# Kernel optimization log

Measured on AMD Instinct MI355X. Metric: run time of the kernel, lower is better.

The kernel has to match this reference:

```python
import jax, jax.numpy as jnp
import numpy as np

DIM = 2048        # model hidden size
INTER = 1408      # per-expert intermediate size
E = 16            # n_routed_experts
TOPK = 2          # n_activated_experts
S_INTER = 2816    # shared experts intermediate (n_shared_experts * INTER)
T = 4096          # tokens (batch*seq, module flattens to [-1, dim])
ROUTE_SCALE = 1.0


def setup_inputs() -> dict:
    key = jax.random.key(0)
    ks = jax.random.split(key, 8)
    g = lambda k, shape, scale: (jax.random.normal(k, shape, dtype=jnp.float32) * scale)
    return {
        "x": g(ks[0], (T, DIM), 1.0),
        "gate_w": g(ks[1], (E, DIM), 0.02),
        "w1": g(ks[2], (E, INTER, DIM), 0.02),
        "w2": g(ks[3], (E, DIM, INTER), 0.02),
        "w3": g(ks[4], (E, INTER, DIM), 0.02),
        "sw1": g(ks[5], (S_INTER, DIM), 0.02),
        "sw2": g(ks[6], (DIM, S_INTER), 0.02),
        "sw3": g(ks[7], (S_INTER, DIM), 0.02),
    }


def _moe_forward(x, gate_w, w1, w2, w3, sw1, sw2, sw3):
    t = x.shape[0]
    # ---- gate: softmax scores -> top-k experts per token ----
    scores = jax.nn.softmax(x @ gate_w.T, axis=-1)          # [T, E]
    top_w, top_i = jax.lax.top_k(scores, TOPK)              # [T, K]
    top_w = top_w * ROUTE_SCALE
    # dense combine weights [T, E]: zero for unselected experts
    combine = jnp.zeros((t, E), x.dtype).at[jnp.arange(t)[:, None], top_i].add(top_w)
    # ---- routed experts: gated silu MLP per expert, weighted combine ----
    # loop over the small fixed expert count; tokens with combine==0 contribute 0,
    # matching the original scatter/gather dispatch math exactly.
    y = jnp.zeros_like(x)
    for e in range(E):
        h = jax.nn.silu(x @ w1[e].T) * (x @ w3[e].T)        # [T, INTER]
        y = y + (h @ w2[e].T) * combine[:, e:e + 1]
    # ---- shared experts ----
    z = (jax.nn.silu(x @ sw1.T) * (x @ sw3.T)) @ sw2.T      # [T, DIM]
    return y + z


def reference(x, gate_w, w1, w2, w3, sw1, sw2, sw3):
    return _moe_forward(x, gate_w, w1, w2, w3, sw1, sw2, sw3)
```

## Files before the change

kernel.cpp:

```cpp
#include <hip/hip_runtime.h>
#include <hip/hip_bf16.h>
#include <cstdint>
#include <cstddef>

#define TTOK   4096
#define DIM_   2048
#define INTER_ 1408
#define NEXP   16
#define SINTER_ 2816
#define BM 128
#define BN 128
#define BK 32
#define MAXROWS (TTOK*2 + NEXP*BM)
#define MAXMT   (TTOK*2/BM + NEXP)

typedef unsigned short u16;
typedef __attribute__((ext_vector_type(8))) short short8;
typedef __attribute__((ext_vector_type(4))) float f32x4;

__device__ __forceinline__ u16 f2bf(float f) {
    __hip_bfloat16 h = __float2bfloat16(f);
    union { __hip_bfloat16 h; u16 u; } c; c.h = h; return c.u;
}

__device__ __forceinline__ unsigned pk2(float a, float b) {
    unsigned r;
    asm("v_cvt_pk_bf16_f32 %0, %1, %2" : "=v"(r) : "v"(a), "v"(b));
    return r;
}

__device__ __forceinline__ int4 pack8(float4 a, float4 b) {
    int4 r;
    r.x = (int)pk2(a.x, a.y);
    r.y = (int)pk2(a.z, a.w);
    r.z = (int)pk2(b.x, b.y);
    r.w = (int)pk2(b.z, b.w);
    return r;
}


__global__ void init_kernel(int* perm_rt, float* pw_rt, int* perm_sh, int* misc) {
    int i = blockIdx.x * 256 + threadIdx.x;
    if (i < MAXROWS) { perm_rt[i] = -1; pw_rt[i] = 0.f; }
    if (i < TTOK)    perm_sh[i] = i;
    if (i < 32)      misc[i] = 0;
}

__global__ void convert_x_kernel(const float* __restrict__ x, u16* __restrict__ xb) {
    size_t i = (size_t)blockIdx.x * 256 + threadIdx.x;
    float4 v = *(const float4*)(x + i * 4);
    uint2 o;
    o.x = pk2(v.x, v.y);
    o.y = pk2(v.z, v.w);
    *(uint2*)(xb + i * 4) = o;
}

__global__ void gate_kernel(const float* __restrict__ x, const float* __restrict__ gw,
                            int* __restrict__ topi, float* __restrict__ topw,
                            int* __restrict__ misc) {
    int t = blockIdx.x;
    int lane = threadIdx.x;
    const float* xr = x + (size_t)t * DIM_;
    float acc[NEXP];
#pragma unroll
    for (int e = 0; e < NEXP; e++) acc[e] = 0.f;
#pragma unroll
    for (int i = 0; i < 8; i++) {
        int k = i * 256 + lane * 4;
        float4 xv = *(const float4*)(xr + k);
#pragma unroll
        for (int e = 0; e < NEXP; e++) {
            float4 gv = *(const float4*)(gw + (size_t)e * DIM_ + k);
            acc[e] += xv.x * gv.x + xv.y * gv.y + xv.z * gv.z + xv.w * gv.w;
        }
    }
#pragma unroll
    for (int e = 0; e < NEXP; e++) {
        float v = acc[e];
        for (int off = 32; off > 0; off >>= 1) v += __shfl_down(v, off);
        acc[e] = v;
    }
    if (lane == 0) {
        float m = acc[0];
#pragma unroll
        for (int e = 1; e < NEXP; e++) m = fmaxf(m, acc[e]);
        float p[NEXP]; float s = 0.f;
#pragma unroll
        for (int e = 0; e < NEXP; e++) { p[e] = __expf(acc[e] - m); s += p[e]; }
        int i0 = 0; float v0 = p[0];
#pragma unroll
        for (int e = 1; e < NEXP; e++) if (p[e] > v0) { v0 = p[e]; i0 = e; }
        int i1 = -1; float v1 = -1.f;
#pragma unroll
        for (int e = 0; e < NEXP; e++) if (e != i0 && p[e] > v1) { v1 = p[e]; i1 = e; }
        float inv = 1.f / s;
        topi[2 * t] = i0; topi[2 * t + 1] = i1;
        topw[2 * t] = v0 * inv; topw[2 * t + 1] = v1 * inv;
        atomicAdd(&misc[i0], 1);
        atomicAdd(&misc[i1], 1);
    }
}

__global__ void scan_kernel(int* misc) {
    int* counts = misc;
    int* base   = misc + 32;
    int* te     = misc + 48;
    int* tr     = misc + 128;
    int b = 0, tt = 0;
    for (int e = 0; e < NEXP; e++) {
        int c = counts[e];
        int nt = (c + BM - 1) >> 7;
        base[e] = b;
        for (int i = 0; i < nt; i++) { te[tt] = e; tr[tt] = b + i * BM; tt++; }
        b += nt * BM;
    }
    for (int i = tt; i < MAXMT; i++) te[i] = -1;
}

__global__ void scatter_kernel(const int* __restrict__ topi, const float* __restrict__ topw,
                               int* __restrict__ misc, int* __restrict__ perm,
                               float* __restrict__ pw) {
    int t = blockIdx.x * 256 + threadIdx.x;
    if (t >= TTOK) return;
    int* fill = misc + 16;
    int* base = misc + 32;
#pragma unroll
    for (int k = 0; k < 2; k++) {
        int e = topi[2 * t + k];
        int pos = base[e] + atomicAdd(&fill[e], 1);
        perm[pos] = t;
        pw[pos] = topw[2 * t + k];
    }
}


template<bool GROUPED>
__global__ __launch_bounds__(256, 2) void gemm_h13_k(
    const u16* __restrict__ Xb,
    const float* __restrict__ W1b, const float* __restrict__ W3b,
    u16* __restrict__ H,
    const int* __restrict__ perm,
    const int* __restrict__ te, const int* __restrict__ tr,
    int N, int K, int nt_m, int chunk)
{
    const int q = (blockIdx.x & 7) * chunk + (blockIdx.x >> 3);
    if (q >= nt_m * (N / BN)) return;
    const int jn = q / nt_m, im = q % nt_m;
    int e, slot0;
    if (GROUPED) { e = te[im]; if (e < 0) return; slot0 = tr[im]; }
    else         { e = 0; slot0 = im * BM; }
    const int n0 = jn * BN;
    const float* W1 = W1b + (size_t)e * N * K;
    const float* W3 = W3b + (size_t)e * N * K;

    __shared__ __align__(16) u16 As[BM * BK];
    __shared__ __align__(16) u16 B1s[BM * BK];
    __shared__ __align__(16) u16 B3s[BM * BK];

    const int tid = threadIdx.x;
    const int lane = tid & 63, wid = tid >> 6;
    const int wr = wid >> 1, wc = wid & 1;
    const int col = lane & 15, kg = lane >> 4;

    const int r0 = tid >> 2, ko = (tid & 3) * 8;
    const int tok0 = perm[slot0 + r0];
    const int tok1 = perm[slot0 + r0 + 64];
    const u16* pA0 = (tok0 >= 0) ? Xb + (size_t)tok0 * K + ko : nullptr;
    const u16* pA1 = (tok1 >= 0) ? Xb + (size_t)tok1 * K + ko : nullptr;
    const int rB = tid >> 1, hfB = (tid & 1) * 16;
    const float* p1 = W1 + (size_t)(n0 + rB) * K + hfB;
    const float* p3 = W3 + (size_t)(n0 + rB) * K + hfB;

    f32x4 acc1[4][4] = {};
    f32x4 acc3[4][4] = {};

    int4 va0, va1;
    float4 f1[4], f3[4];

    va0 = pA0 ? *(const int4*)(pA0) : make_int4(0, 0, 0, 0);
    va1 = pA1 ? *(const int4*)(pA1) : make_int4(0, 0, 0, 0);
#pragma unroll
    for (int i = 0; i < 4; i++) { f1[i] = *(const float4*)(p1 + i * 4); f3[i] = *(const float4*)(p3 + i * 4); }

    for (int k0 = 0; k0 < K; k0 += BK) {
        *(int4*)(As + r0 * BK + ko) = va0;
        *(int4*)(As + (r0 + 64) * BK + ko) = va1;
        *(int4*)(B1s + rB * BK + hfB)     = pack8(f1[0], f1[1]);
        *(int4*)(B1s + rB * BK + hfB + 8) = pack8(f1[2], f1[3]);
        *(int4*)(B3s + rB * BK + hfB)     = pack8(f3[0], f3[1]);
        *(int4*)(B3s + rB * BK + hfB + 8) = pack8(f3[2], f3[3]);
        __syncthreads();

        const int kn = k0 + BK;
        if (kn < K) {
            va0 = pA0 ? *(const int4*)(pA0 + kn) : make_int4(0, 0, 0, 0);
            va1 = pA1 ? *(const int4*)(pA1 + kn) : make_int4(0, 0, 0, 0);
#pragma unroll
            for (int i = 0; i < 4; i++) {
                f1[i] = *(const float4*)(p1 + kn + i * 4);
                f3[i] = *(const float4*)(p3 + kn + i * 4);
            }
        }

        short8 a[4];
#pragma unroll
        for (int mi = 0; mi < 4; mi++)
            a[mi] = *(const short8*)(As + (wr * 64 + mi * 16 + col) * BK + kg * 8);
#pragma unroll
        for (int ni = 0; ni < 4; ni++) {
            short8 v1 = *(const short8*)(B1s + (wc * 64 + ni * 16 + col) * BK + kg * 8);
            short8 v3 = *(const short8*)(B3s + (wc * 64 + ni * 16 + col) * BK + kg * 8);
#pragma unroll
            for (int mi = 0; mi < 4; mi++) {
                acc1[mi][ni] = __builtin_amdgcn_mfma_f32_16x16x32_bf16(a[mi], v1, acc1[mi][ni], 0, 0, 0);
                acc3[mi][ni] = __builtin_amdgcn_mfma_f32_16x16x32_bf16(a[mi], v3, acc3[mi][ni], 0, 0, 0);
            }
        }
        __syncthreads();
    }

#pragma unroll
    for (int mi = 0; mi < 4; mi++) {
#pragma unroll
        for (int j = 0; j < 4; j++) {
            int row = slot0 + wr * 64 + mi * 16 + kg * 4 + j;
#pragma unroll
            for (int ni = 0; ni < 4; ni++) {
                float v1 = acc1[mi][ni][j];
                float v3 = acc3[mi][ni][j];
                float hv = v1 / (1.f + __expf(-v1)) * v3;
                int c = n0 + wc * 64 + ni * 16 + col;
                H[(size_t)row * N + c] = f2bf(hv);
            }
        }
    }
}

template<bool ATOMIC>
__global__ __launch_bounds__(256, 2) void gemm_out_k(
    const u16* __restrict__ Hm,
    const float* __restrict__ W2b,
    float* __restrict__ Out,
    const int* __restrict__ perm, const float* __restrict__ pw,
    const int* __restrict__ te, const int* __restrict__ tr,
    int K, int nt_m, int chunk)
{
    const int q = (blockIdx.x & 7) * chunk + (blockIdx.x >> 3);
    if (q >= nt_m * (DIM_ / BN)) return;
    const int jn = q / nt_m, im = q % nt_m;
    int e, slot0;
    if (ATOMIC) { e = te[im]; if (e < 0) return; slot0 = tr[im]; }
    else        { e = 0; slot0 = im * BM; }
    const int n0 = jn * BN;
    const float* W2 = W2b + (size_t)e * DIM_ * K;

    __shared__ __align__(16) u16 As[BM * BK];
    __shared__ __align__(16) u16 Bs[BM * BK];

    const int tid = threadIdx.x;
    const int lane = tid & 63, wid = tid >> 6;
    const int wr = wid >> 1, wc = wid & 1;
    const int col = lane & 15, kg = lane >> 4;

    const int r0 = tid >> 2, ko = (tid & 3) * 8;
    const int rB = tid >> 1, hfB = (tid & 1) * 16;
    const u16* pA0 = Hm + (size_t)(slot0 + r0) * K + ko;
    const u16* pA1 = Hm + (size_t)(slot0 + r0 + 64) * K + ko;
    const float* p2 = W2 + (size_t)(n0 + rB) * K + hfB;

    f32x4 acc[4][4] = {};

    int4 va0, va1;
    float4 fb[4];
    va0 = *(const int4*)(pA0);
    va1 = *(const int4*)(pA1);
#pragma unroll
    for (int i = 0; i < 4; i++) fb[i] = *(const float4*)(p2 + i * 4);

    for (int k0 = 0; k0 < K; k0 += BK) {
        *(int4*)(As + r0 * BK + ko) = va0;
        *(int4*)(As + (r0 + 64) * BK + ko) = va1;
        *(int4*)(Bs + rB * BK + hfB)     = pack8(fb[0], fb[1]);
        *(int4*)(Bs + rB * BK + hfB + 8) = pack8(fb[2], fb[3]);
        __syncthreads();

        const int kn = k0 + BK;
        if (kn < K) {
            va0 = *(const int4*)(pA0 + kn);
            va1 = *(const int4*)(pA1 + kn);
#pragma unroll
            for (int i = 0; i < 4; i++) fb[i] = *(const float4*)(p2 + kn + i * 4);
        }

        short8 a[4];
#pragma unroll
        for (int mi = 0; mi < 4; mi++)
            a[mi] = *(const short8*)(As + (wr * 64 + mi * 16 + col) * BK + kg * 8);
#pragma unroll
        for (int ni = 0; ni < 4; ni++) {
            short8 bv = *(const short8*)(Bs + (wc * 64 + ni * 16 + col) * BK + kg * 8);
#pragma unroll
            for (int mi = 0; mi < 4; mi++)
                acc[mi][ni] = __builtin_amdgcn_mfma_f32_16x16x32_bf16(a[mi], bv, acc[mi][ni], 0, 0, 0);
        }
        __syncthreads();
    }

#pragma unroll
    for (int mi = 0; mi < 4; mi++) {
#pragma unroll
        for (int j = 0; j < 4; j++) {
            int rloc = wr * 64 + mi * 16 + kg * 4 + j;
            int slot = slot0 + rloc;
            if (ATOMIC) {
                int token = perm[slot];
                if (token < 0) continue;
                float w = pw[slot];
#pragma unroll
                for (int ni = 0; ni < 4; ni++) {
                    int c = n0 + wc * 64 + ni * 16 + col;
                    atomicAdd(&Out[(size_t)token * DIM_ + c], acc[mi][ni][j] * w);
                }
            } else {
#pragma unroll
                for (int ni = 0; ni < 4; ni++) {
                    int c = n0 + wc * 64 + ni * 16 + col;
                    Out[(size_t)slot * DIM_ + c] = acc[mi][ni][j];
                }
            }
        }
    }
}


extern "C" void kernel_launch(void* const* d_in, const int* in_sizes, int n_in,
                              void* d_out, int out_size, void* d_ws, size_t ws_size,
                              hipStream_t stream) {
    (void)in_sizes; (void)n_in; (void)out_size; (void)ws_size;
    const float* x   = (const float*)d_in[0];
    const float* gw  = (const float*)d_in[1];
    const float* w1  = (const float*)d_in[2];
    const float* w2  = (const float*)d_in[3];
    const float* w3  = (const float*)d_in[4];
    const float* sw1 = (const float*)d_in[5];
    const float* sw2 = (const float*)d_in[6];
    const float* sw3 = (const float*)d_in[7];
    float* out = (float*)d_out;

    char* ws = (char*)d_ws;
    size_t off = 0;
    auto take = [&](size_t bytes) -> void* {
        void* p = ws + off;
        off += (bytes + 255) & ~(size_t)255;
        return p;
    };
    u16*   xb      = (u16*)take((size_t)TTOK * DIM_ * 2);
    u16*   hbuf    = (u16*)take((size_t)MAXROWS * INTER_ * 2);
    int*   perm_rt = (int*)take((size_t)MAXROWS * 4);
    float* pw_rt   = (float*)take((size_t)MAXROWS * 4);
    int*   perm_sh = (int*)take((size_t)TTOK * 4);
    int*   topi    = (int*)take((size_t)TTOK * 2 * 4);
    float* topw    = (float*)take((size_t)TTOK * 2 * 4);
    int*   misc    = (int*)take(1024);

    init_kernel<<<MAXROWS / 256, 256, 0, stream>>>(perm_rt, pw_rt, perm_sh, misc);
    convert_x_kernel<<<(TTOK * DIM_ / 4) / 256, 256, 0, stream>>>(x, xb);
    gate_kernel<<<TTOK, 64, 0, stream>>>(x, gw, topi, topw, misc);
    scan_kernel<<<1, 1, 0, stream>>>(misc);
    scatter_kernel<<<TTOK / 256, 256, 0, stream>>>(topi, topw, misc, perm_rt, pw_rt);

    auto grid8 = [](int total) { return ((total + 7) / 8) * 8; };
    auto chunk8 = [](int total) { return (total + 7) / 8; };

    {
        int total = (TTOK / BM) * (SINTER_ / BN);
        gemm_h13_k<false><<<grid8(total), 256, 0, stream>>>(
            xb, sw1, sw3, hbuf, perm_sh, nullptr, nullptr, SINTER_, DIM_, TTOK / BM, chunk8(total));
    }
    {
        int total = (TTOK / BM) * (DIM_ / BN);
        gemm_out_k<false><<<grid8(total), 256, 0, stream>>>(
            hbuf, sw2, out, nullptr, nullptr, nullptr, nullptr, SINTER_, TTOK / BM, chunk8(total));
    }
    {
        int total = MAXMT * (INTER_ / BN);
        gemm_h13_k<true><<<grid8(total), 256, 0, stream>>>(
            xb, w1, w3, hbuf, perm_rt, misc + 48, misc + 128, INTER_, DIM_, MAXMT, chunk8(total));
    }
    {
        int total = MAXMT * (DIM_ / BN);
        gemm_out_k<true><<<grid8(total), 256, 0, stream>>>(
            hbuf, w2, out, perm_rt, pw_rt, misc + 48, misc + 128, INTER_, MAXMT, chunk8(total));
    }
}
```

Before: 868.7 us.

## Pre-convert weights to bf16 and stage GEMM tiles via global_load_lds

Adds a bulk pass that converts all expert and shared weights from fp32 to bf16 in workspace on every call. New GEMM kernels then read bf16 weights and use global_load_lds to copy A/B tiles straight into shared memory, replacing the register-staged fp32 load and in-loop pack. A zero row stands in for padded tokens so the direct loads never need a null check. The weight conversion adds a full fp32 read plus bf16 write of every weight on each call. The new loop is single-buffered with no prefetch overlap, and the old fp32 path is kept as a fallback when the workspace is too small.

```diff
diff --git a/kernel.cpp b/kernel.cpp
--- a/kernel.cpp
+++ b/kernel.cpp
@@ -18,6 +18,13 @@
 typedef __attribute__((ext_vector_type(8))) short short8;
 typedef __attribute__((ext_vector_type(4))) float f32x4;
 
+#define AS3P(p) ((__attribute__((address_space(3))) void*)(p))
+#define AS1P(p) ((const __attribute__((address_space(1))) void*)(p))
+
+__device__ __forceinline__ void gll16(const u16* g, u16* l) {
+    __builtin_amdgcn_global_load_lds(AS1P(g), AS3P(l), 16, 0, 0);
+}
+
 __device__ __forceinline__ u16 f2bf(float f) {
     __hip_bfloat16 h = __float2bfloat16(f);
     union { __hip_bfloat16 h; u16 u; } c; c.h = h; return c.u;
@@ -39,20 +46,21 @@
 }
 
 
-__global__ void init_kernel(int* perm_rt, float* pw_rt, int* perm_sh, int* misc) {
+__global__ void init_kernel(int* perm_rt, float* pw_rt, int* perm_sh, int* misc, int* zrow) {
     int i = blockIdx.x * 256 + threadIdx.x;
     if (i < MAXROWS) { perm_rt[i] = -1; pw_rt[i] = 0.f; }
     if (i < TTOK)    perm_sh[i] = i;
     if (i < 32)      misc[i] = 0;
-}
-
-__global__ void convert_x_kernel(const float* __restrict__ x, u16* __restrict__ xb) {
-    size_t i = (size_t)blockIdx.x * 256 + threadIdx.x;
-    float4 v = *(const float4*)(x + i * 4);
-    uint2 o;
-    o.x = pk2(v.x, v.y);
-    o.y = pk2(v.z, v.w);
-    *(uint2*)(xb + i * 4) = o;
+    if (i < 1024)    zrow[i] = 0;
+}
+
+__global__ void cvt_kernel(const float* __restrict__ s, u16* __restrict__ d, int n8) {
+    int stride = gridDim.x * 256;
+    for (int i = blockIdx.x * 256 + threadIdx.x; i < n8; i += stride) {
+        const float4* s4 = (const float4*)(s + (size_t)i * 8);
+        float4 a = s4[0], b = s4[1];
+        *(int4*)(d + (size_t)i * 8) = pack8(a, b);
+    }
 }
 
 __global__ void gate_kernel(const float* __restrict__ x, const float* __restrict__ gw,
@@ -136,6 +144,185 @@
 
 template<bool GROUPED>
 __global__ __launch_bounds__(256, 2) void gemm_h13_k(
+    const u16* __restrict__ Xb,
+    const u16* __restrict__ W1b, const u16* __restrict__ W3b,
+    u16* __restrict__ H,
+    const int* __restrict__ perm,
+    const int* __restrict__ te, const int* __restrict__ tr,
+    const u16* __restrict__ zrow,
+    int N, int K, int nt_m, int chunk)
+{
+    const int q = (blockIdx.x & 7) * chunk + (blockIdx.x >> 3);
+    if (q >= nt_m * (N / BN)) return;
+    const int jn = q / nt_m, im = q % nt_m;
+    int e, slot0;
+    if (GROUPED) { e = te[im]; if (e < 0) return; slot0 = tr[im]; }
+    else         { e = 0; slot0 = im * BM; }
+    const int n0 = jn * BN;
+    const u16* W1 = W1b + (size_t)e * N * K;
+    const u16* W3 = W3b + (size_t)e * N * K;
+
+    __shared__ __align__(16) u16 As[BM * BK];
+    __shared__ __align__(16) u16 B1s[BM * BK];
+    __shared__ __align__(16) u16 B3s[BM * BK];
+
+    const int tid = threadIdx.x;
+    const int lane = tid & 63, wid = tid >> 6;
+    const int wr = wid >> 1, wc = wid & 1;
+    const int col = lane & 15, kg = lane >> 4;
+
+    const int lr = lane >> 2, kb = (lane & 3) * 8;
+    const int ar0 = wid * 32 + lr, ar1 = ar0 + 16;
+    const int ta0 = perm[slot0 + ar0];
+    const int ta1 = perm[slot0 + ar1];
+    const u16* ga0 = (ta0 >= 0 ? Xb + (size_t)ta0 * K : zrow) + kb;
+    const u16* ga1 = (ta1 >= 0 ? Xb + (size_t)ta1 * K : zrow) + kb;
+    const u16* gb1a = W1 + (size_t)(n0 + ar0) * K + kb;
+    const u16* gb1b = W1 + (size_t)(n0 + ar1) * K + kb;
+    const u16* gb3a = W3 + (size_t)(n0 + ar0) * K + kb;
+    const u16* gb3b = W3 + (size_t)(n0 + ar1) * K + kb;
+    u16* la0 = As  + (wid * 32) * BK;
+    u16* la1 = As  + (wid * 32 + 16) * BK;
+    u16* lb1a = B1s + (wid * 32) * BK;
+    u16* lb1b = B1s + (wid * 32 + 16) * BK;
+    u16* lb3a = B3s + (wid * 32) * BK;
+    u16* lb3b = B3s + (wid * 32 + 16) * BK;
+
+    f32x4 acc1[4][4] = {};
+    f32x4 acc3[4][4] = {};
+
+    for (int k0 = 0; k0 < K; k0 += BK) {
+        gll16(ga0 + k0, la0);
+        gll16(ga1 + k0, la1);
+        gll16(gb1a + k0, lb1a);
+        gll16(gb1b + k0, lb1b);
+        gll16(gb3a + k0, lb3a);
+        gll16(gb3b + k0, lb3b);
+        __syncthreads();
+
+        short8 a[4];
+#pragma unroll
+        for (int mi = 0; mi < 4; mi++)
+            a[mi] = *(const short8*)(As + (wr * 64 + mi * 16 + col) * BK + kg * 8);
+#pragma unroll
+        for (int ni = 0; ni < 4; ni++) {
+            short8 v1 = *(const short8*)(B1s + (wc * 64 + ni * 16 + col) * BK + kg * 8);
+            short8 v3 = *(const short8*)(B3s + (wc * 64 + ni * 16 + col) * BK + kg * 8);
+#pragma unroll
+            for (int mi = 0; mi < 4; mi++) {
+                acc1[mi][ni] = __builtin_amdgcn_mfma_f32_16x16x32_bf16(a[mi], v1, acc1[mi][ni], 0, 0, 0);
+                acc3[mi][ni] = __builtin_amdgcn_mfma_f32_16x16x32_bf16(a[mi], v3, acc3[mi][ni], 0, 0, 0);
+            }
+        }
+        __syncthreads();
+    }
+
+#pragma unroll
+    for (int mi = 0; mi < 4; mi++) {
+#pragma unroll
+        for (int j = 0; j < 4; j++) {
+            int row = slot0 + wr * 64 + mi * 16 + kg * 4 + j;
+#pragma unroll
+            for (int ni = 0; ni < 4; ni++) {
+                float v1 = acc1[mi][ni][j];
+                float v3 = acc3[mi][ni][j];
+                float hv = v1 / (1.f + __expf(-v1)) * v3;
+                int c = n0 + wc * 64 + ni * 16 + col;
+                H[(size_t)row * N + c] = f2bf(hv);
+            }
+        }
+    }
+}
+
+template<bool ATOMIC>
+__global__ __launch_bounds__(256, 2) void gemm_out_k(
+    const u16* __restrict__ Hm,
+    const u16* __restrict__ W2b,
+    float* __restrict__ Out,
+    const int* __restrict__ perm, const float* __restrict__ pw,
+    const int* __restrict__ te, const int* __restrict__ tr,
+    int K, int nt_m, int chunk)
+{
+    const int q = (blockIdx.x & 7) * chunk + (blockIdx.x >> 3);
+    if (q >= nt_m * (DIM_ / BN)) return;
+    const int jn = q / nt_m, im = q % nt_m;
+    int e, slot0;
+    if (ATOMIC) { e = te[im]; if (e < 0) return; slot0 = tr[im]; }
+    else        { e = 0; slot0 = im * BM; }
+    const int n0 = jn * BN;
+    const u16* W2 = W2b + (size_t)e * DIM_ * K;
+
+    __shared__ __align__(16) u16 As[BM * BK];
+    __shared__ __align__(16) u16 Bs[BM * BK];
+
+    const int tid = threadIdx.x;
+    const int lane = tid & 63, wid = tid >> 6;
+    const int wr = wid >> 1, wc = wid & 1;
+    const int col = lane & 15, kg = lane >> 4;
+
+    const int lr = lane >> 2, kb = (lane & 3) * 8;
+    const int ar0 = wid * 32 + lr, ar1 = ar0 + 16;
+    const u16* ga0 = Hm + (size_t)(slot0 + ar0) * K + kb;
+    const u16* ga1 = Hm + (size_t)(slot0 + ar1) * K + kb;
+    const u16* gb0 = W2 + (size_t)(n0 + ar0) * K + kb;
+    const u16* gb1 = W2 + (size_t)(n0 + ar1) * K + kb;
+    u16* la0 = As + (wid * 32) * BK;
+    u16* la1 = As + (wid * 32 + 16) * BK;
+    u16* lb0 = Bs + (wid * 32) * BK;
+    u16* lb1 = Bs + (wid * 32 + 16) * BK;
+
+    f32x4 acc[4][4] = {};
+
+    for (int k0 = 0; k0 < K; k0 += BK) {
+        gll16(ga0 + k0, la0);
+        gll16(ga1 + k0, la1);
+        gll16(gb0 + k0, lb0);
+        gll16(gb1 + k0, lb1);
+        __syncthreads();
+
+        short8 a[4];
+#pragma unroll
+        for (int mi = 0; mi < 4; mi++)
+            a[mi] = *(const short8*)(As + (wr * 64 + mi * 16 + col) * BK + kg * 8);
+#pragma unroll
+        for (int ni = 0; ni < 4; ni++) {
+            short8 bv = *(const short8*)(Bs + (wc * 64 + ni * 16 + col) * BK + kg * 8);
+#pragma unroll
+            for (int mi = 0; mi < 4; mi++)
+                acc[mi][ni] = __builtin_amdgcn_mfma_f32_16x16x32_bf16(a[mi], bv, acc[mi][ni], 0, 0, 0);
+        }
+        __syncthreads();
+    }
+
+#pragma unroll
+    for (int mi = 0; mi < 4; mi++) {
+#pragma unroll
+        for (int j = 0; j < 4; j++) {
+            int rloc = wr * 64 + mi * 16 + kg * 4 + j;
+            int slot = slot0 + rloc;
+            if (ATOMIC) {
+                int token = perm[slot];
+                if (token < 0) continue;
+                float w = pw[slot];
+#pragma unroll
+                for (int ni = 0; ni < 4; ni++) {
+                    int c = n0 + wc * 64 + ni * 16 + col;
+                    atomicAdd(&Out[(size_t)token * DIM_ + c], acc[mi][ni][j] * w);
+                }
+            } else {
+#pragma unroll
+                for (int ni = 0; ni < 4; ni++) {
+                    int c = n0 + wc * 64 + ni * 16 + col;
+                    Out[(size_t)slot * DIM_ + c] = acc[mi][ni][j];
+                }
+            }
+        }
+    }
+}
+
+
+template<bool GROUPED>
+__global__ __launch_bounds__(256, 2) void gemm_h13_f32(
     const u16* __restrict__ Xb,
     const float* __restrict__ W1b, const float* __restrict__ W3b,
     u16* __restrict__ H,
@@ -176,7 +363,6 @@
 
     int4 va0, va1;
     float4 f1[4], f3[4];
-
     va0 = pA0 ? *(const int4*)(pA0) : make_int4(0, 0, 0, 0);
     va1 = pA1 ? *(const int4*)(pA1) : make_int4(0, 0, 0, 0);
 #pragma unroll
@@ -237,7 +423,7 @@
 }
 
 template<bool ATOMIC>
-__global__ __launch_bounds__(256, 2) void gemm_out_k(
+__global__ __launch_bounds__(256, 2) void gemm_out_f32(
     const u16* __restrict__ Hm,
     const float* __restrict__ W2b,
     float* __restrict__ Out,
@@ -336,7 +522,7 @@
 extern "C" void kernel_launch(void* const* d_in, const int* in_sizes, int n_in,
                               void* d_out, int out_size, void* d_ws, size_t ws_size,
                               hipStream_t stream) {
-    (void)in_sizes; (void)n_in; (void)out_size; (void)ws_size;
+    (void)in_sizes; (void)n_in; (void)out_size;
     const float* x   = (const float*)d_in[0];
     const float* gw  = (const float*)d_in[1];
     const float* w1  = (const float*)d_in[2];
@@ -362,9 +548,21 @@
     int*   topi    = (int*)take((size_t)TTOK * 2 * 4);
     float* topw    = (float*)take((size_t)TTOK * 2 * 4);
     int*   misc    = (int*)take(1024);
-
-    init_kernel<<<MAXROWS / 256, 256, 0, stream>>>(perm_rt, pw_rt, perm_sh, misc);
-    convert_x_kernel<<<(TTOK * DIM_ / 4) / 256, 256, 0, stream>>>(x, xb);
+    int*   zrow    = (int*)take(4096);
+    const size_t nW  = (size_t)NEXP * INTER_ * DIM_;
+    const size_t nSW = (size_t)SINTER_ * DIM_;
+    size_t common_end = off;
+    u16* w1b  = (u16*)take(nW * 2);
+    u16* w2b  = (u16*)take(nW * 2);
+    u16* w3b  = (u16*)take(nW * 2);
+    u16* sw1b = (u16*)take(nSW * 2);
+    u16* sw2b = (u16*)take(nSW * 2);
+    u16* sw3b = (u16*)take(nSW * 2);
+    const bool fast = (off <= ws_size);
+    (void)common_end;
+
+    init_kernel<<<MAXROWS / 256, 256, 0, stream>>>(perm_rt, pw_rt, perm_sh, misc, zrow);
+    cvt_kernel<<<2048, 256, 0, stream>>>(x, xb, TTOK * DIM_ / 8);
     gate_kernel<<<TTOK, 64, 0, stream>>>(x, gw, topi, topw, misc);
     scan_kernel<<<1, 1, 0, stream>>>(misc);
     scatter_kernel<<<TTOK / 256, 256, 0, stream>>>(topi, topw, misc, perm_rt, pw_rt);
@@ -372,24 +570,58 @@
     auto grid8 = [](int total) { return ((total + 7) / 8) * 8; };
     auto chunk8 = [](int total) { return (total + 7) / 8; };
 
-    {
-        int total = (TTOK / BM) * (SINTER_ / BN);
-        gemm_h13_k<false><<<grid8(total), 256, 0, stream>>>(
-            xb, sw1, sw3, hbuf, perm_sh, nullptr, nullptr, SINTER_, DIM_, TTOK / BM, chunk8(total));
-    }
-    {
-        int total = (TTOK / BM) * (DIM_ / BN);
-        gemm_out_k<false><<<grid8(total), 256, 0, stream>>>(
-            hbuf, sw2, out, nullptr, nullptr, nullptr, nullptr, SINTER_, TTOK / BM, chunk8(total));
-    }
-    {
-        int total = MAXMT * (INTER_ / BN);
-        gemm_h13_k<true><<<grid8(total), 256, 0, stream>>>(
-            xb, w1, w3, hbuf, perm_rt, misc + 48, misc + 128, INTER_, DIM_, MAXMT, chunk8(total));
-    }
-    {
-        int total = MAXMT * (DIM_ / BN);
-        gemm_out_k<true><<<grid8(total), 256, 0, stream>>>(
-            hbuf, w2, out, perm_rt, pw_rt, misc + 48, misc + 128, INTER_, MAXMT, chunk8(total));
-    }
-}
+    if (fast) {
+        cvt_kernel<<<2048, 256, 0, stream>>>(w1,  w1b,  (int)(nW / 8));
+        cvt_kernel<<<2048, 256, 0, stream>>>(w2,  w2b,  (int)(nW / 8));
+        cvt_kernel<<<2048, 256, 0, stream>>>(w3,  w3b,  (int)(nW / 8));
+        cvt_kernel<<<2048, 256, 0, stream>>>(sw1, sw1b, (int)(nSW / 8));
+        cvt_kernel<<<2048, 256, 0, stream>>>(sw2, sw2b, (int)(nSW / 8));
+        cvt_kernel<<<2048, 256, 0, stream>>>(sw3, sw3b, (int)(nSW / 8));
+
+        {
+            int total = (TTOK / BM) * (SINTER_ / BN);
+            gemm_h13_k<false><<<grid8(total), 256, 0, stream>>>(
+                xb, sw1b, sw3b, hbuf, perm_sh, nullptr, nullptr, (const u16*)zrow,
+                SINTER_, DIM_, TTOK / BM, chunk8(total));
+        }
+        {
+            int total = (TTOK / BM) * (DIM_ / BN);
+            gemm_out_k<false><<<grid8(total), 256, 0, stream>>>(
+                hbuf, sw2b, out, nullptr, nullptr, nullptr, nullptr,
+                SINTER_, TTOK / BM, chunk8(total));
+        }
+        {
+            int total = MAXMT * (INTER_ / BN);
+            gemm_h13_k<true><<<grid8(total), 256, 0, stream>>>(
+                xb, w1b, w3b, hbuf, perm_rt, misc + 48, misc + 128, (const u16*)zrow,
+                INTER_, DIM_, MAXMT, chunk8(total));
+        }
+        {
+            int total = MAXMT * (DIM_ / BN);
+            gemm_out_k<true><<<grid8(total), 256, 0, stream>>>(
+                hbuf, w2b, out, perm_rt, pw_rt, misc + 48, misc + 128,
+                INTER_, MAXMT, chunk8(total));
+        }
+    } else {
+        {
+            int total = (TTOK / BM) * (SINTER_ / BN);
+            gemm_h13_f32<false><<<grid8(total), 256, 0, stream>>>(
+                xb, sw1, sw3, hbuf, perm_sh, nullptr, nullptr, SINTER_, DIM_, TTOK / BM, chunk8(total));
+        }
+        {
+            int total = (TTOK / BM) * (DIM_ / BN);
+            gemm_out_f32<false><<<grid8(total), 256, 0, stream>>>(
+                hbuf, sw2, out, nullptr, nullptr, nullptr, nullptr, SINTER_, TTOK / BM, chunk8(total));
+        }
+        {
+            int total = MAXMT * (INTER_ / BN);
+            gemm_h13_f32<true><<<grid8(total), 256, 0, stream>>>(
+                xb, w1, w3, hbuf, perm_rt, misc + 48, misc + 128, INTER_, DIM_, MAXMT, chunk8(total));
+        }
+        {
+            int total = MAXMT * (DIM_ / BN);
+            gemm_out_f32<true><<<grid8(total), 256, 0, stream>>>(
+                hbuf, w2, out, perm_rt, pw_rt, misc + 48, misc + 128, INTER_, MAXMT, chunk8(total));
+        }
+    }
+}
```

New measurement: 871.6 us. Within noise of the previous version (+0.3%).

## Load GEMM tiles via direct global-to-LDS DMA with swizzled fp32 weight staging

Applied to the files above, without the earlier changes.

Both GEMM kernels now move A and B tiles into LDS with global_load_lds instructions instead of register staging. Weights stay fp32 in LDS and are converted to bf16 at fragment-read time. XOR swizzles are added to reduce LDS bank conflicts, and a zero row in memory replaces the null-pointer padding for unfilled slots. The change also drops the register-prefetch double buffering, so loads are no longer overlapped with MFMA work. LDS per block grows because the fp32 B tiles are larger, and launch bounds are raised to 4 blocks per SM.

```diff
diff --git a/kernel.cpp b/kernel.cpp
--- a/kernel.cpp
+++ b/kernel.cpp
@@ -18,6 +18,13 @@
 typedef __attribute__((ext_vector_type(8))) short short8;
 typedef __attribute__((ext_vector_type(4))) float f32x4;
 
+#define AS3P(p) ((__attribute__((address_space(3))) void*)(p))
+#define AS1P(p) ((const __attribute__((address_space(1))) void*)(p))
+
+__device__ __forceinline__ void gll16(const void* g, void* l) {
+    __builtin_amdgcn_global_load_lds(AS1P(g), AS3P(l), 16, 0, 0);
+}
+
 __device__ __forceinline__ u16 f2bf(float f) {
     __hip_bfloat16 h = __float2bfloat16(f);
     union { __hip_bfloat16 h; u16 u; } c; c.h = h; return c.u;
@@ -27,6 +34,13 @@
     unsigned r;
     asm("v_cvt_pk_bf16_f32 %0, %1, %2" : "=v"(r) : "v"(a), "v"(b));
     return r;
+}
+
+__device__ __forceinline__ short8 cvt8(float4 q0, float4 q1) {
+    union { int4 i; short8 s; } u;
+    u.i = make_int4((int)pk2(q0.x, q0.y), (int)pk2(q0.z, q0.w),
+                    (int)pk2(q1.x, q1.y), (int)pk2(q1.z, q1.w));
+    return u.s;
 }
 
 __device__ __forceinline__ int4 pack8(float4 a, float4 b) {
@@ -39,20 +53,21 @@
 }
 
 
-__global__ void init_kernel(int* perm_rt, float* pw_rt, int* perm_sh, int* misc) {
+__global__ void init_kernel(int* perm_rt, float* pw_rt, int* perm_sh, int* misc, int* zrow) {
     int i = blockIdx.x * 256 + threadIdx.x;
     if (i < MAXROWS) { perm_rt[i] = -1; pw_rt[i] = 0.f; }
     if (i < TTOK)    perm_sh[i] = i;
     if (i < 32)      misc[i] = 0;
-}
-
-__global__ void convert_x_kernel(const float* __restrict__ x, u16* __restrict__ xb) {
-    size_t i = (size_t)blockIdx.x * 256 + threadIdx.x;
-    float4 v = *(const float4*)(x + i * 4);
-    uint2 o;
-    o.x = pk2(v.x, v.y);
-    o.y = pk2(v.z, v.w);
-    *(uint2*)(xb + i * 4) = o;
+    if (i < 1024)    zrow[i] = 0;
+}
+
+__global__ void cvt_kernel(const float* __restrict__ s, u16* __restrict__ d, int n8) {
+    int stride = gridDim.x * 256;
+    for (int i = blockIdx.x * 256 + threadIdx.x; i < n8; i += stride) {
+        const float4* s4 = (const float4*)(s + (size_t)i * 8);
+        float4 a = s4[0], b = s4[1];
+        *(int4*)(d + (size_t)i * 8) = pack8(a, b);
+    }
 }
 
 __global__ void gate_kernel(const float* __restrict__ x, const float* __restrict__ gw,
@@ -135,12 +150,13 @@
 
 
 template<bool GROUPED>
-__global__ __launch_bounds__(256, 2) void gemm_h13_k(
+__global__ __launch_bounds__(256, 4) void gemm_h13_k(
     const u16* __restrict__ Xb,
     const float* __restrict__ W1b, const float* __restrict__ W3b,
     u16* __restrict__ H,
     const int* __restrict__ perm,
     const int* __restrict__ te, const int* __restrict__ tr,
+    const u16* __restrict__ zrow,
     int N, int K, int nt_m, int chunk)
 {
     const int q = (blockIdx.x & 7) * chunk + (blockIdx.x >> 3);
@@ -153,63 +169,60 @@
     const float* W1 = W1b + (size_t)e * N * K;
     const float* W3 = W3b + (size_t)e * N * K;
 
-    __shared__ __align__(16) u16 As[BM * BK];
-    __shared__ __align__(16) u16 B1s[BM * BK];
-    __shared__ __align__(16) u16 B3s[BM * BK];
+    __shared__ __align__(16) u16   As[BM * BK];
+    __shared__ __align__(16) float B1f[BM * BK];
+    __shared__ __align__(16) float B3f[BM * BK];
 
     const int tid = threadIdx.x;
     const int lane = tid & 63, wid = tid >> 6;
     const int wr = wid >> 1, wc = wid & 1;
     const int col = lane & 15, kg = lane >> 4;
 
-    const int r0 = tid >> 2, ko = (tid & 3) * 8;
-    const int tok0 = perm[slot0 + r0];
-    const int tok1 = perm[slot0 + r0 + 64];
-    const u16* pA0 = (tok0 >= 0) ? Xb + (size_t)tok0 * K + ko : nullptr;
-    const u16* pA1 = (tok1 >= 0) ? Xb + (size_t)tok1 * K + ko : nullptr;
-    const int rB = tid >> 1, hfB = (tid & 1) * 16;
-    const float* p1 = W1 + (size_t)(n0 + rB) * K + hfB;
-    const float* p3 = W3 + (size_t)(n0 + rB) * K + hfB;
+    const int aRow = wid * 32 + (lane >> 2);
+    const int aCk  = ((lane & 3) ^ ((lane >> 3) & 3)) * 8;
+    const int ta0 = perm[slot0 + aRow];
+    const int ta1 = perm[slot0 + aRow + 16];
+    const u16* ga0 = (ta0 >= 0 ? Xb + (size_t)ta0 * K : zrow) + aCk;
+    const u16* ga1 = (ta1 >= 0 ? Xb + (size_t)ta1 * K : zrow) + aCk;
+    u16* la0 = As + (wid * 32) * BK;
+    u16* la1 = As + (wid * 32 + 16) * BK;
+
+    const int bRowL = lane >> 3;
+    const int bCk   = ((lane & 7) ^ bRowL) * 4;
+    const float* g1 = W1 + (size_t)(n0 + wid * 32 + bRowL) * K + bCk;
+    const float* g3 = W3 + (size_t)(n0 + wid * 32 + bRowL) * K + bCk;
+    float* lb1 = B1f + (wid * 32) * BK;
+    float* lb3 = B3f + (wid * 32) * BK;
+
+    const int aswz = (col >> 1) & 3;
+    const int bswz = col & 7;
 
     f32x4 acc1[4][4] = {};
     f32x4 acc3[4][4] = {};
 
-    int4 va0, va1;
-    float4 f1[4], f3[4];
-
-    va0 = pA0 ? *(const int4*)(pA0) : make_int4(0, 0, 0, 0);
-    va1 = pA1 ? *(const int4*)(pA1) : make_int4(0, 0, 0, 0);
-#pragma unroll
-    for (int i = 0; i < 4; i++) { f1[i] = *(const float4*)(p1 + i * 4); f3[i] = *(const float4*)(p3 + i * 4); }
-
     for (int k0 = 0; k0 < K; k0 += BK) {
-        *(int4*)(As + r0 * BK + ko) = va0;
-        *(int4*)(As + (r0 + 64) * BK + ko) = va1;
-        *(int4*)(B1s + rB * BK + hfB)     = pack8(f1[0], f1[1]);
-        *(int4*)(B1s + rB * BK + hfB + 8) = pack8(f1[2], f1[3]);
-        *(int4*)(B3s + rB * BK + hfB)     = pack8(f3[0], f3[1]);
-        *(int4*)(B3s + rB * BK + hfB + 8) = pack8(f3[2], f3[3]);
+        gll16(ga0 + k0, la0);
+        gll16(ga1 + k0, la1);
+#pragma unroll
+        for (int j = 0; j < 4; j++) {
+            gll16(g1 + (size_t)j * 8 * K + k0, lb1 + j * 8 * BK);
+            gll16(g3 + (size_t)j * 8 * K + k0, lb3 + j * 8 * BK);
+        }
         __syncthreads();
 
-        const int kn = k0 + BK;
-        if (kn < K) {
-            va0 = pA0 ? *(const int4*)(pA0 + kn) : make_int4(0, 0, 0, 0);
-            va1 = pA1 ? *(const int4*)(pA1 + kn) : make_int4(0, 0, 0, 0);
-#pragma unroll
-            for (int i = 0; i < 4; i++) {
-                f1[i] = *(const float4*)(p1 + kn + i * 4);
-                f3[i] = *(const float4*)(p3 + kn + i * 4);
-            }
-        }
-
         short8 a[4];
 #pragma unroll
         for (int mi = 0; mi < 4; mi++)
-            a[mi] = *(const short8*)(As + (wr * 64 + mi * 16 + col) * BK + kg * 8);
+            a[mi] = *(const short8*)(As + (wr * 64 + mi * 16 + col) * BK + ((kg ^ aswz) * 8));
 #pragma unroll
         for (int ni = 0; ni < 4; ni++) {
-            short8 v1 = *(const short8*)(B1s + (wc * 64 + ni * 16 + col) * BK + kg * 8);
-            short8 v3 = *(const short8*)(B3s + (wc * 64 + ni * 16 + col) * BK + kg * 8);
+            const int rowB = wc * 64 + ni * 16 + col;
+            const float* rb1 = B1f + rowB * BK;
+            const float* rb3 = B3f + rowB * BK;
+            const int c0 = ((kg * 2) ^ bswz) * 4;
+            const int c1 = ((kg * 2 + 1) ^ bswz) * 4;
+            short8 v1 = cvt8(*(const float4*)(rb1 + c0), *(const float4*)(rb1 + c1));
+            short8 v3 = cvt8(*(const float4*)(rb3 + c0), *(const float4*)(rb3 + c1));
 #pragma unroll
             for (int mi = 0; mi < 4; mi++) {
                 acc1[mi][ni] = __builtin_amdgcn_mfma_f32_16x16x32_bf16(a[mi], v1, acc1[mi][ni], 0, 0, 0);
@@ -237,7 +250,7 @@
 }
 
 template<bool ATOMIC>
-__global__ __launch_bounds__(256, 2) void gemm_out_k(
+__global__ __launch_bounds__(256, 4) void gemm_out_k(
     const u16* __restrict__ Hm,
     const float* __restrict__ W2b,
     float* __restrict__ Out,
@@ -254,51 +267,50 @@
     const int n0 = jn * BN;
     const float* W2 = W2b + (size_t)e * DIM_ * K;
 
-    __shared__ __align__(16) u16 As[BM * BK];
-    __shared__ __align__(16) u16 Bs[BM * BK];
+    __shared__ __align__(16) u16   As[BM * BK];
+    __shared__ __align__(16) float Bf[BM * BK];
 
     const int tid = threadIdx.x;
     const int lane = tid & 63, wid = tid >> 6;
     const int wr = wid >> 1, wc = wid & 1;
     const int col = lane & 15, kg = lane >> 4;
 
-    const int r0 = tid >> 2, ko = (tid & 3) * 8;
-    const int rB = tid >> 1, hfB = (tid & 1) * 16;
-    const u16* pA0 = Hm + (size_t)(slot0 + r0) * K + ko;
-    const u16* pA1 = Hm + (size_t)(slot0 + r0 + 64) * K + ko;
-    const float* p2 = W2 + (size_t)(n0 + rB) * K + hfB;
+    const int aRow = wid * 32 + (lane >> 2);
+    const int aCk  = ((lane & 3) ^ ((lane >> 3) & 3)) * 8;
+    const u16* ga0 = Hm + (size_t)(slot0 + aRow) * K + aCk;
+    const u16* ga1 = Hm + (size_t)(slot0 + aRow + 16) * K + aCk;
+    u16* la0 = As + (wid * 32) * BK;
+    u16* la1 = As + (wid * 32 + 16) * BK;
+
+    const int bRowL = lane >> 3;
+    const int bCk   = ((lane & 7) ^ bRowL) * 4;
+    const float* g2 = W2 + (size_t)(n0 + wid * 32 + bRowL) * K + bCk;
+    float* lb = Bf + (wid * 32) * BK;
+
+    const int aswz = (col >> 1) & 3;
+    const int bswz = col & 7;
 
     f32x4 acc[4][4] = {};
 
-    int4 va0, va1;
-    float4 fb[4];
-    va0 = *(const int4*)(pA0);
-    va1 = *(const int4*)(pA1);
-#pragma unroll
-    for (int i = 0; i < 4; i++) fb[i] = *(const float4*)(p2 + i * 4);
-
     for (int k0 = 0; k0 < K; k0 += BK) {
-        *(int4*)(As + r0 * BK + ko) = va0;
-        *(int4*)(As + (r0 + 64) * BK + ko) = va1;
-        *(int4*)(Bs + rB * BK + hfB)     = pack8(fb[0], fb[1]);
-        *(int4*)(Bs + rB * BK + hfB + 8) = pack8(fb[2], fb[3]);
+        gll16(ga0 + k0, la0);
+        gll16(ga1 + k0, la1);
+#pragma unroll
+        for (int j = 0; j < 4; j++)
+            gll16(g2 + (size_t)j * 8 * K + k0, lb + j * 8 * BK);
         __syncthreads();
 
-        const int kn = k0 + BK;
-        if (kn < K) {
-            va0 = *(const int4*)(pA0 + kn);
-            va1 = *(const int4*)(pA1 + kn);
-#pragma unroll
-            for (int i = 0; i < 4; i++) fb[i] = *(const float4*)(p2 + kn + i * 4);
-        }
-
         short8 a[4];
 #pragma unroll
         for (int mi = 0; mi < 4; mi++)
-            a[mi] = *(const short8*)(As + (wr * 64 + mi * 16 + col) * BK + kg * 8);
+            a[mi] = *(const short8*)(As + (wr * 64 + mi * 16 + col) * BK + ((kg ^ aswz) * 8));
 #pragma unroll
         for (int ni = 0; ni < 4; ni++) {
-            short8 bv = *(const short8*)(Bs + (wc * 64 + ni * 16 + col) * BK + kg * 8);
+            const int rowB = wc * 64 + ni * 16 + col;
+            const float* rb = Bf + rowB * BK;
+            const int c0 = ((kg * 2) ^ bswz) * 4;
+            const int c1 = ((kg * 2 + 1) ^ bswz) * 4;
+            short8 bv = cvt8(*(const float4*)(rb + c0), *(const float4*)(rb + c1));
 #pragma unroll
             for (int mi = 0; mi < 4; mi++)
                 acc[mi][ni] = __builtin_amdgcn_mfma_f32_16x16x32_bf16(a[mi], bv, acc[mi][ni], 0, 0, 0);
@@ -362,9 +374,10 @@
     int*   topi    = (int*)take((size_t)TTOK * 2 * 4);
     float* topw    = (float*)take((size_t)TTOK * 2 * 4);
     int*   misc    = (int*)take(1024);
-
-    init_kernel<<<MAXROWS / 256, 256, 0, stream>>>(perm_rt, pw_rt, perm_sh, misc);
-    convert_x_kernel<<<(TTOK * DIM_ / 4) / 256, 256, 0, stream>>>(x, xb);
+    int*   zrow    = (int*)take(4096);
+
+    init_kernel<<<MAXROWS / 256, 256, 0, stream>>>(perm_rt, pw_rt, perm_sh, misc, zrow);
+    cvt_kernel<<<512, 256, 0, stream>>>(x, xb, TTOK * DIM_ / 8);
     gate_kernel<<<TTOK, 64, 0, stream>>>(x, gw, topi, topw, misc);
     scan_kernel<<<1, 1, 0, stream>>>(misc);
     scatter_kernel<<<TTOK / 256, 256, 0, stream>>>(topi, topw, misc, perm_rt, pw_rt);
@@ -375,21 +388,25 @@
     {
         int total = (TTOK / BM) * (SINTER_ / BN);
         gemm_h13_k<false><<<grid8(total), 256, 0, stream>>>(
-            xb, sw1, sw3, hbuf, perm_sh, nullptr, nullptr, SINTER_, DIM_, TTOK / BM, chunk8(total));
+            xb, sw1, sw3, hbuf, perm_sh, nullptr, nullptr, (const u16*)zrow,
+            SINTER_, DIM_, TTOK / BM, chunk8(total));
     }
     {
         int total = (TTOK / BM) * (DIM_ / BN);
         gemm_out_k<false><<<grid8(total), 256, 0, stream>>>(
-            hbuf, sw2, out, nullptr, nullptr, nullptr, nullptr, SINTER_, TTOK / BM, chunk8(total));
+            hbuf, sw2, out, nullptr, nullptr, nullptr, nullptr,
+            SINTER_, TTOK / BM, chunk8(total));
     }
     {
         int total = MAXMT * (INTER_ / BN);
         gemm_h13_k<true><<<grid8(total), 256, 0, stream>>>(
-            xb, w1, w3, hbuf, perm_rt, misc + 48, misc + 128, INTER_, DIM_, MAXMT, chunk8(total));
+            xb, w1, w3, hbuf, perm_rt, misc + 48, misc + 128, (const u16*)zrow,
+            INTER_, DIM_, MAXMT, chunk8(total));
     }
     {
         int total = MAXMT * (DIM_ / BN);
         gemm_out_k<true><<<grid8(total), 256, 0, stream>>>(
-            hbuf, w2, out, perm_rt, pw_rt, misc + 48, misc + 128, INTER_, MAXMT, chunk8(total));
-    }
-}
+            hbuf, w2, out, perm_rt, pw_rt, misc + 48, misc + 128,
+            INTER_, MAXMT, chunk8(total));
+    }
+}
```

After: 2.806 ms. 3.23x slower.
